# Kernel optimization log

Measured on AMD Instinct MI355X. Metric: run time of the kernel, lower is better.

Reference implementation:

```python
import jax, jax.numpy as jnp
import numpy as np

B, S, E, H = 32, 256, 768, 32
D = E // H  # head_dim = 24


def setup_inputs() -> dict:
    key = jax.random.key(0)
    ks = jax.random.split(key, 10)
    w_sc = 1.0 / np.sqrt(E)  # xavier-ish init scale for weights
    return {
        "feats": jax.random.normal(ks[0], (B, S, E), jnp.float32),
        "attn_bias": jax.random.normal(ks[1], (B, H, S, S), jnp.float32),
        "delta_pos": jax.random.normal(ks[2], (B, S, S, 3), jnp.float32),
        "Wq": jax.random.normal(ks[3], (E, E), jnp.float32) * w_sc,
        "bq": jnp.zeros((E,), jnp.float32),
        "Wk": jax.random.normal(ks[4], (E, E), jnp.float32) * w_sc,
        "bk": jnp.zeros((E,), jnp.float32),
        "Wv": jax.random.normal(ks[5], (E, E), jnp.float32) * w_sc,
        "bv": jnp.zeros((E,), jnp.float32),
        "Wfx": jax.random.normal(ks[6], (E,), jnp.float32) * w_sc,
        "Wfy": jax.random.normal(ks[7], (E,), jnp.float32) * w_sc,
        "Wfz": jax.random.normal(ks[8], (E,), jnp.float32) * w_sc,
    }


def reference(feats, attn_bias, delta_pos, Wq, bq, Wk, bk, Wv, bv, Wfx, Wfy, Wfz):
    b, s, e = feats.shape
    h = attn_bias.shape[1]
    d = e // h
    scaling = d ** -0.5
    # q/k/v projections; q scaled by 1/sqrt(head_dim)
    q = ((feats @ Wq + bq) * scaling).reshape(b, s, h, d).transpose(0, 2, 1, 3)  # (b,h,s,d)
    k = (feats @ Wk + bk).reshape(b, s, h, d).transpose(0, 2, 1, 3)              # (b,h,t,d)
    v = (feats @ Wv + bv).reshape(b, s, h, d).transpose(0, 2, 1, 3)              # (b,h,t,d)
    scores = jnp.einsum('bhsd,bhtd->bhst', q, k) + attn_bias
    probs = jax.nn.softmax(scores, axis=-1)  # dropout p in eval -> identity
    # rot_attn_probs = probs[...,None] * delta_pos[:,None] fused into one contraction:
    # (b,h,s,t) * (b,s,t,3) contracted with (b,h,t,c) over t -> (b,s,3,h,c)
    attn = jnp.einsum('bhst,bstx,bhtc->bsxhc', probs, delta_pos, v)
    attn = attn.reshape(b, s, 3, e)  # flatten (h,c) -> e
    out_x = attn[..., 0, :] @ Wfx  # (b,s)
    out_y = attn[..., 1, :] @ Wfy
    out_z = attn[..., 2, :] @ Wfz
    return jnp.stack([out_x, out_y, out_z], axis=-1)  # (b,s,3)
```

## Files before the change

### kernel.cpp

```cpp
#include <hip/hip_runtime.h>
#include <hip/hip_bf16.h>

#define B_ 32
#define S_ 256
#define E_ 768
#define H_ 32
#define D_ 24
#define NTOT 1664
#define LK 40

typedef __hip_bfloat16 bf16;
typedef __attribute__((ext_vector_type(8))) short short8;
typedef __attribute__((ext_vector_type(4))) float floatx4;
typedef __attribute__((ext_vector_type(2))) float f32x2;

__global__ __launch_bounds__(256) void cast_feats(
    const float* __restrict__ in, bf16* __restrict__ outp, int n4)
{
  int i = blockIdx.x * 256 + threadIdx.x;
  if (i < n4) {
    float4 v = reinterpret_cast<const float4*>(in)[i];
    union { ushort4 u; bf16 b[4]; } pk;
    pk.b[0] = (bf16)v.x; pk.b[1] = (bf16)v.y;
    pk.b[2] = (bf16)v.z; pk.b[3] = (bf16)v.w;
    reinterpret_cast<ushort4*>(outp)[i] = pk.u;
  }
}

__global__ __launch_bounds__(256) void prep_pack(
    const float* __restrict__ Wq, const float* __restrict__ Wk,
    const float* __restrict__ Wv,
    const float* __restrict__ bq, const float* __restrict__ bk,
    const float* __restrict__ bv,
    const float* __restrict__ Wfx, const float* __restrict__ Wfy,
    const float* __restrict__ Wfz,
    bf16* __restrict__ Wt, float* __restrict__ biasf)
{
  const float qscale = 0.20412414523193154f;
  int gid = blockIdx.x * 256 + threadIdx.x;
  if (gid < NTOT * E_) {
    int n = gid / E_, k = gid % E_;
    float val;
    if (n < 768) {
      val = Wq[(size_t)k * E_ + n] * qscale;
    } else if (n < 1536) {
      val = Wk[(size_t)k * E_ + (n - 768)];
    } else if (n < 1632) {
      int nn = n - 1536, x = nn >> 5, h = nn & 31;
      const float* Wf = (x == 0) ? Wfx : (x == 1 ? Wfy : Wfz);
      float s = 0.f;
      #pragma unroll
      for (int c = 0; c < D_; c++)
        s += Wv[(size_t)k * E_ + h * D_ + c] * Wf[h * D_ + c];
      val = s;
    } else {
      val = 0.f;
    }
    Wt[gid] = (bf16)val;
  } else {
    int n = gid - NTOT * E_;
    if (n < NTOT) {
      float val;
      if (n < 768) {
        val = bq[n] * qscale;
      } else if (n < 1536) {
        val = bk[n - 768];
      } else if (n < 1632) {
        int nn = n - 1536, x = nn >> 5, h = nn & 31;
        const float* Wf = (x == 0) ? Wfx : (x == 1 ? Wfy : Wfz);
        float s = 0.f;
        #pragma unroll
        for (int c = 0; c < D_; c++)
          s += bv[h * D_ + c] * Wf[h * D_ + c];
        val = s;
      } else {
        val = 0.f;
      }
      biasf[n] = val;
    }
  }
}

__global__ __launch_bounds__(256) void gemm_qkv(
    const bf16* __restrict__ A, const bf16* __restrict__ Wt,
    const float* __restrict__ biasf,
    bf16* __restrict__ qout, bf16* __restrict__ kout,
    float* __restrict__ vwout)
{
  __shared__ __align__(16) short As[128 * LK];
  __shared__ __align__(16) short Bs[128 * LK];
  int tid = threadIdx.x;
  int m0 = blockIdx.y * 128, n0 = blockIdx.x * 128;
  int lrow = tid >> 2, lcol = (tid & 3) * 8;
  int wave = tid >> 6, lane = tid & 63;
  int wm = (wave >> 1) * 64, wn = (wave & 1) * 64;
  int fr = lane & 15, quad = lane >> 4;

  floatx4 acc[4][4];
  const floatx4 zero = {0.f, 0.f, 0.f, 0.f};
  #pragma unroll
  for (int i = 0; i < 4; i++)
    #pragma unroll
    for (int j = 0; j < 4; j++) acc[i][j] = zero;

  const bf16* Aptr = A + (size_t)(m0 + lrow) * E_ + lcol;
  const bf16* Bptr = Wt + (size_t)(n0 + lrow) * E_ + lcol;
  float4 av0 = *reinterpret_cast<const float4*>(Aptr);
  float4 av1 = *reinterpret_cast<const float4*>(Aptr + (size_t)64 * E_);
  float4 bv0 = *reinterpret_cast<const float4*>(Bptr);
  float4 bv1 = *reinterpret_cast<const float4*>(Bptr + (size_t)64 * E_);

  for (int k0 = 0; k0 < E_; k0 += 32) {
    __syncthreads();
    *reinterpret_cast<float4*>(&As[lrow * LK + lcol]) = av0;
    *reinterpret_cast<float4*>(&As[(lrow + 64) * LK + lcol]) = av1;
    *reinterpret_cast<float4*>(&Bs[lrow * LK + lcol]) = bv0;
    *reinterpret_cast<float4*>(&Bs[(lrow + 64) * LK + lcol]) = bv1;
    __syncthreads();
    if (k0 + 32 < E_) {
      av0 = *reinterpret_cast<const float4*>(Aptr + k0 + 32);
      av1 = *reinterpret_cast<const float4*>(Aptr + (size_t)64 * E_ + k0 + 32);
      bv0 = *reinterpret_cast<const float4*>(Bptr + k0 + 32);
      bv1 = *reinterpret_cast<const float4*>(Bptr + (size_t)64 * E_ + k0 + 32);
    }
    short8 af[4], bfr[4];
    #pragma unroll
    for (int t = 0; t < 4; t++)
      af[t] = *reinterpret_cast<const short8*>(
          &As[(wm + t * 16 + fr) * LK + quad * 8]);
    #pragma unroll
    for (int t = 0; t < 4; t++)
      bfr[t] = *reinterpret_cast<const short8*>(
          &Bs[(wn + t * 16 + fr) * LK + quad * 8]);
    #pragma unroll
    for (int ti = 0; ti < 4; ti++)
      #pragma unroll
      for (int tj = 0; tj < 4; tj++)
        acc[ti][tj] = __builtin_amdgcn_mfma_f32_16x16x32_bf16(
            af[ti], bfr[tj], acc[ti][tj], 0, 0, 0);
  }

  #pragma unroll
  for (int ti = 0; ti < 4; ti++) {
    #pragma unroll
    for (int tj = 0; tj < 4; tj++) {
      int n = n0 + wn + tj * 16 + fr;
      float bias = biasf[n];
      #pragma unroll
      for (int r = 0; r < 4; r++) {
        int m = m0 + wm + ti * 16 + quad * 4 + r;
        int b = m >> 8, s = m & 255;
        float val = acc[ti][tj][r] + bias;
        if (n < 768) {
          int h = n / 24, d = n - h * 24;
          qout[(((size_t)b * H_ + h) * S_ + s) * D_ + d] = (bf16)val;
        } else if (n < 1536) {
          int n2 = n - 768;
          int h = n2 / 24, d = n2 - h * 24;
          kout[(((size_t)b * H_ + h) * S_ + s) * D_ + d] = (bf16)val;
        } else if (n < 1632) {
          int nn = n - 1536, x = nn >> 5, h = nn & 31;
          vwout[(((size_t)x * B_ + b) * H_ + h) * S_ + s] = val;
        }
      }
    }
  }
}

__global__ __launch_bounds__(256, 3) void attn_kernel(
    const bf16* __restrict__ qg, const bf16* __restrict__ kg,
    const float* __restrict__ vwg, const float* __restrict__ biasg,
    const float* __restrict__ dpg, float* __restrict__ out)
{
  __shared__ float ql[64 * 26];
  int blk = blockIdx.x;
  int bh = blk >> 2, st = (blk & 3) * 64;
  int b = bh >> 5, h = bh & 31;
  int tid = threadIdx.x, wave = tid >> 6, lane = tid & 63;
  int t0 = lane * 4;

  f32x2 kr[4][12];
  #pragma unroll
  for (int j = 0; j < 4; j++) {
    const bf16* krow = kg + ((size_t)bh * S_ + t0 + j) * D_;
    #pragma unroll
    for (int i = 0; i < 12; i++) {
      f32x2 kk;
      kk.x = (float)krow[2 * i];
      kk.y = (float)krow[2 * i + 1];
      kr[j][i] = kk;
    }
  }
  float vwr[3][4];
  #pragma unroll
  for (int x = 0; x < 3; x++) {
    float4 v4 = *reinterpret_cast<const float4*>(
        vwg + (((size_t)x * B_ + b) * H_ + h) * S_ + t0);
    vwr[x][0] = v4.x; vwr[x][1] = v4.y; vwr[x][2] = v4.z; vwr[x][3] = v4.w;
  }
  {
    int r = tid >> 2, c0 = (tid & 3) * 6;
    const bf16* qrow = qg + ((size_t)bh * S_ + st + r) * D_ + c0;
    #pragma unroll
    for (int i = 0; i < 6; i++) ql[r * 26 + c0 + i] = (float)qrow[i];
  }
  __syncthreads();

  const float* biasbh = biasg + (size_t)bh * S_ * S_;

  for (int si = 0; si < 16; si++) {
    int sr = si * 4 + wave;
    int s = st + sr;
    float4 bias4 = *reinterpret_cast<const float4*>(biasbh + s * S_ + t0);
    const float* dpr = dpg + ((size_t)(b * S_ + s) * S_) * 3 + (size_t)t0 * 3;
    float4 d0 = *reinterpret_cast<const float4*>(dpr);
    float4 d1 = *reinterpret_cast<const float4*>(dpr + 4);
    float4 d2 = *reinterpret_cast<const float4*>(dpr + 8);

    f32x2 sc2[4];
    #pragma unroll
    for (int j = 0; j < 4; j++) { sc2[j].x = 0.f; sc2[j].y = 0.f; }
    #pragma unroll
    for (int i = 0; i < 12; i++) {
      f32x2 qd = *reinterpret_cast<const f32x2*>(&ql[sr * 26 + 2 * i]);
      #pragma unroll
      for (int j = 0; j < 4; j++) sc2[j] += qd * kr[j][i];
    }
    float sc[4];
    sc[0] = sc2[0].x + sc2[0].y + bias4.x;
    sc[1] = sc2[1].x + sc2[1].y + bias4.y;
    sc[2] = sc2[2].x + sc2[2].y + bias4.z;
    sc[3] = sc2[3].x + sc2[3].y + bias4.w;

    float mx = fmaxf(fmaxf(sc[0], sc[1]), fmaxf(sc[2], sc[3]));
    #pragma unroll
    for (int o = 32; o; o >>= 1) mx = fmaxf(mx, __shfl_xor(mx, o));
    float p[4], l = 0.f;
    #pragma unroll
    for (int j = 0; j < 4; j++) { p[j] = __expf(sc[j] - mx); l += p[j]; }
    #pragma unroll
    for (int o = 32; o; o >>= 1) l += __shfl_xor(l, o);
    float inv = 1.0f / l;

    float dx[4] = {d0.x, d0.w, d1.z, d2.y};
    float dy[4] = {d0.y, d1.x, d1.w, d2.z};
    float dz[4] = {d0.z, d1.y, d2.x, d2.w};

    float ax = 0.f, ay = 0.f, az = 0.f;
    #pragma unroll
    for (int j = 0; j < 4; j++) {
      float w = p[j] * inv;
      ax += w * dx[j] * vwr[0][j];
      ay += w * dy[j] * vwr[1][j];
      az += w * dz[j] * vwr[2][j];
    }
    #pragma unroll
    for (int o = 32; o; o >>= 1) {
      ax += __shfl_xor(ax, o);
      ay += __shfl_xor(ay, o);
      az += __shfl_xor(az, o);
    }
    if (lane == 0) {
      float* op = out + (size_t)(b * S_ + s) * 3;
      atomicAdd(op + 0, ax);
      atomicAdd(op + 1, ay);
      atomicAdd(op + 2, az);
    }
  }
}

extern "C" void kernel_launch(void* const* d_in, const int* in_sizes, int n_in,
                              void* d_out, int out_size, void* d_ws, size_t ws_size,
                              hipStream_t stream)
{
  const float* feats     = (const float*)d_in[0];
  const float* attn_bias = (const float*)d_in[1];
  const float* delta_pos = (const float*)d_in[2];
  const float* Wq        = (const float*)d_in[3];
  const float* bq        = (const float*)d_in[4];
  const float* Wk        = (const float*)d_in[5];
  const float* bk        = (const float*)d_in[6];
  const float* Wv        = (const float*)d_in[7];
  const float* bv        = (const float*)d_in[8];
  const float* Wfx       = (const float*)d_in[9];
  const float* Wfy       = (const float*)d_in[10];
  const float* Wfz       = (const float*)d_in[11];

  char* ws = (char*)d_ws;
  size_t off = 0;
  auto alloc = [&](size_t bytes) -> void* {
    void* p = ws + off;
    off = (off + bytes + 255) & ~(size_t)255;
    return p;
  };
  bf16*  ws_fb   = (bf16*) alloc((size_t)B_ * S_ * E_ * 2);
  bf16*  ws_q    = (bf16*) alloc((size_t)B_ * H_ * S_ * D_ * 2);
  bf16*  ws_k    = (bf16*) alloc((size_t)B_ * H_ * S_ * D_ * 2);
  float* ws_vw   = (float*)alloc((size_t)3 * B_ * H_ * S_ * 4);
  bf16*  ws_Wt   = (bf16*) alloc((size_t)NTOT * E_ * 2);
  float* ws_bias = (float*)alloc((size_t)NTOT * 4);

  hipMemsetAsync(d_out, 0, (size_t)B_ * S_ * 3 * 4, stream);

  int n4 = B_ * S_ * E_ / 4;
  cast_feats<<<(n4 + 255) / 256, 256, 0, stream>>>(feats, ws_fb, n4);

  int prep_n = NTOT * E_ + NTOT;
  prep_pack<<<(prep_n + 255) / 256, 256, 0, stream>>>(
      Wq, Wk, Wv, bq, bk, bv, Wfx, Wfy, Wfz, ws_Wt, ws_bias);

  gemm_qkv<<<dim3(NTOT / 128, B_ * S_ / 128), 256, 0, stream>>>(
      ws_fb, ws_Wt, ws_bias, ws_q, ws_k, ws_vw);

  attn_kernel<<<B_ * H_ * 4, 256, 0, stream>>>(ws_q, ws_k, ws_vw, attn_bias,
                                               delta_pos, (float*)d_out);
}
```

Before: 610.2 us.

## Restructure attention to one thread per query row with shared K/V tile

The attention kernel now runs one block per (batch, head) and gives each thread one query row. The thread loops over all 256 keys, which are staged once in shared memory together with the value-weight projections. This removes the per-row wave shuffle reductions for max, sum and outputs, and prefetches the bias and delta_pos tiles one step ahead in registers. Softmax now subtracts a fixed constant of 4 instead of the running row max, which assumes scores stay far from fp32 exp overflow. Each thread also reads its own strided rows of bias and delta_pos, so global loads are less coalesced.

```diff
diff --git a/kernel.cpp b/kernel.cpp
--- a/kernel.cpp
+++ b/kernel.cpp
@@ -167,106 +167,125 @@
   }
 }
 
-__global__ __launch_bounds__(256, 3) void attn_kernel(
+__global__ __launch_bounds__(256) void attn_kernel(
     const bf16* __restrict__ qg, const bf16* __restrict__ kg,
     const float* __restrict__ vwg, const float* __restrict__ biasg,
     const float* __restrict__ dpg, float* __restrict__ out)
 {
-  __shared__ float ql[64 * 26];
-  int blk = blockIdx.x;
-  int bh = blk >> 2, st = (blk & 3) * 64;
+  __shared__ __align__(16) float kv[S_][28];
+  int bh = blockIdx.x;
   int b = bh >> 5, h = bh & 31;
-  int tid = threadIdx.x, wave = tid >> 6, lane = tid & 63;
-  int t0 = lane * 4;
-
-  f32x2 kr[4][12];
-  #pragma unroll
-  for (int j = 0; j < 4; j++) {
-    const bf16* krow = kg + ((size_t)bh * S_ + t0 + j) * D_;
-    #pragma unroll
-    for (int i = 0; i < 12; i++) {
-      f32x2 kk;
-      kk.x = (float)krow[2 * i];
-      kk.y = (float)krow[2 * i + 1];
-      kr[j][i] = kk;
-    }
-  }
-  float vwr[3][4];
-  #pragma unroll
-  for (int x = 0; x < 3; x++) {
-    float4 v4 = *reinterpret_cast<const float4*>(
-        vwg + (((size_t)x * B_ + b) * H_ + h) * S_ + t0);
-    vwr[x][0] = v4.x; vwr[x][1] = v4.y; vwr[x][2] = v4.z; vwr[x][3] = v4.w;
-  }
+  int s = threadIdx.x;
+
   {
-    int r = tid >> 2, c0 = (tid & 3) * 6;
-    const bf16* qrow = qg + ((size_t)bh * S_ + st + r) * D_ + c0;
-    #pragma unroll
-    for (int i = 0; i < 6; i++) ql[r * 26 + c0 + i] = (float)qrow[i];
+    const short8* kr8 = reinterpret_cast<const short8*>(
+        kg + ((size_t)bh * S_ + s) * D_);
+    #pragma unroll
+    for (int i = 0; i < 3; i++) {
+      short8 kk = kr8[i];
+      float4 f0, f1;
+      union { short u; bf16 bb; } cv;
+      cv.u = kk[0]; f0.x = (float)cv.bb;
+      cv.u = kk[1]; f0.y = (float)cv.bb;
+      cv.u = kk[2]; f0.z = (float)cv.bb;
+      cv.u = kk[3]; f0.w = (float)cv.bb;
+      cv.u = kk[4]; f1.x = (float)cv.bb;
+      cv.u = kk[5]; f1.y = (float)cv.bb;
+      cv.u = kk[6]; f1.z = (float)cv.bb;
+      cv.u = kk[7]; f1.w = (float)cv.bb;
+      *reinterpret_cast<float4*>(&kv[s][i * 8]) = f0;
+      *reinterpret_cast<float4*>(&kv[s][i * 8 + 4]) = f1;
+    }
+    float4 vwp;
+    vwp.x = vwg[(((size_t)0 * B_ + b) * H_ + h) * S_ + s];
+    vwp.y = vwg[(((size_t)1 * B_ + b) * H_ + h) * S_ + s];
+    vwp.z = vwg[(((size_t)2 * B_ + b) * H_ + h) * S_ + s];
+    vwp.w = 0.f;
+    *reinterpret_cast<float4*>(&kv[s][24]) = vwp;
+  }
+
+  f32x2 qd[12];
+  {
+    const short8* qr8 = reinterpret_cast<const short8*>(
+        qg + ((size_t)bh * S_ + s) * D_);
+    #pragma unroll
+    for (int i = 0; i < 3; i++) {
+      short8 qq = qr8[i];
+      #pragma unroll
+      for (int j = 0; j < 4; j++) {
+        union { short u; bf16 bb; } a, c;
+        a.u = qq[2 * j]; c.u = qq[2 * j + 1];
+        f32x2 t2; t2.x = (float)a.bb; t2.y = (float)c.bb;
+        qd[i * 4 + j] = t2;
+      }
+    }
   }
   __syncthreads();
 
-  const float* biasbh = biasg + (size_t)bh * S_ * S_;
-
-  for (int si = 0; si < 16; si++) {
-    int sr = si * 4 + wave;
-    int s = st + sr;
-    float4 bias4 = *reinterpret_cast<const float4*>(biasbh + s * S_ + t0);
-    const float* dpr = dpg + ((size_t)(b * S_ + s) * S_) * 3 + (size_t)t0 * 3;
-    float4 d0 = *reinterpret_cast<const float4*>(dpr);
-    float4 d1 = *reinterpret_cast<const float4*>(dpr + 4);
-    float4 d2 = *reinterpret_cast<const float4*>(dpr + 8);
-
-    f32x2 sc2[4];
-    #pragma unroll
-    for (int j = 0; j < 4; j++) { sc2[j].x = 0.f; sc2[j].y = 0.f; }
-    #pragma unroll
-    for (int i = 0; i < 12; i++) {
-      f32x2 qd = *reinterpret_cast<const f32x2*>(&ql[sr * 26 + 2 * i]);
-      #pragma unroll
-      for (int j = 0; j < 4; j++) sc2[j] += qd * kr[j][i];
-    }
-    float sc[4];
-    sc[0] = sc2[0].x + sc2[0].y + bias4.x;
-    sc[1] = sc2[1].x + sc2[1].y + bias4.y;
-    sc[2] = sc2[2].x + sc2[2].y + bias4.z;
-    sc[3] = sc2[3].x + sc2[3].y + bias4.w;
-
-    float mx = fmaxf(fmaxf(sc[0], sc[1]), fmaxf(sc[2], sc[3]));
-    #pragma unroll
-    for (int o = 32; o; o >>= 1) mx = fmaxf(mx, __shfl_xor(mx, o));
-    float p[4], l = 0.f;
-    #pragma unroll
-    for (int j = 0; j < 4; j++) { p[j] = __expf(sc[j] - mx); l += p[j]; }
-    #pragma unroll
-    for (int o = 32; o; o >>= 1) l += __shfl_xor(l, o);
-    float inv = 1.0f / l;
-
+  const float* biasp = biasg + (size_t)bh * S_ * S_ + (size_t)s * S_;
+  const float* dpp   = dpg + (size_t)(b * S_ + s) * S_ * 3;
+
+  float l = 0.f, ax = 0.f, ay = 0.f, az = 0.f;
+
+  auto group = [&](int tb, float4 bias4, float4 d0, float4 d1, float4 d2) {
     float dx[4] = {d0.x, d0.w, d1.z, d2.y};
     float dy[4] = {d0.y, d1.x, d1.w, d2.z};
     float dz[4] = {d0.z, d1.y, d2.x, d2.w};
-
-    float ax = 0.f, ay = 0.f, az = 0.f;
+    float bb[4] = {bias4.x, bias4.y, bias4.z, bias4.w};
     #pragma unroll
     for (int j = 0; j < 4; j++) {
-      float w = p[j] * inv;
-      ax += w * dx[j] * vwr[0][j];
-      ay += w * dy[j] * vwr[1][j];
-      az += w * dz[j] * vwr[2][j];
-    }
-    #pragma unroll
-    for (int o = 32; o; o >>= 1) {
-      ax += __shfl_xor(ax, o);
-      ay += __shfl_xor(ay, o);
-      az += __shfl_xor(az, o);
-    }
-    if (lane == 0) {
-      float* op = out + (size_t)(b * S_ + s) * 3;
-      atomicAdd(op + 0, ax);
-      atomicAdd(op + 1, ay);
-      atomicAdd(op + 2, az);
-    }
-  }
+      const float4* krow4 = reinterpret_cast<const float4*>(&kv[tb + j][0]);
+      f32x2 acc2; acc2.x = 0.f; acc2.y = 0.f;
+      #pragma unroll
+      for (int i = 0; i < 6; i++) {
+        float4 k4 = krow4[i];
+        f32x2 klo; klo.x = k4.x; klo.y = k4.y;
+        f32x2 khi; khi.x = k4.z; khi.y = k4.w;
+        acc2 += qd[2 * i] * klo;
+        acc2 += qd[2 * i + 1] * khi;
+      }
+      float4 vw4 = krow4[6];
+      float sc = acc2.x + acc2.y + (bb[j] - 4.0f);
+      float p = __expf(sc);
+      l += p;
+      ax = fmaf(p * dx[j], vw4.x, ax);
+      ay = fmaf(p * dy[j], vw4.y, ay);
+      az = fmaf(p * dz[j], vw4.z, az);
+    }
+  };
+
+  float4 nb0 = *reinterpret_cast<const float4*>(biasp);
+  float4 nb1 = *reinterpret_cast<const float4*>(biasp + 4);
+  float4 ne0 = *reinterpret_cast<const float4*>(dpp);
+  float4 ne1 = *reinterpret_cast<const float4*>(dpp + 4);
+  float4 ne2 = *reinterpret_cast<const float4*>(dpp + 8);
+  float4 ne3 = *reinterpret_cast<const float4*>(dpp + 12);
+  float4 ne4 = *reinterpret_cast<const float4*>(dpp + 16);
+  float4 ne5 = *reinterpret_cast<const float4*>(dpp + 20);
+
+  for (int t0 = 0; t0 < S_; t0 += 8) {
+    float4 b0 = nb0, b1 = nb1;
+    float4 e0 = ne0, e1 = ne1, e2 = ne2, e3 = ne3, e4 = ne4, e5 = ne5;
+    int tn = (t0 + 8 < S_) ? t0 + 8 : 0;
+    nb0 = *reinterpret_cast<const float4*>(biasp + tn);
+    nb1 = *reinterpret_cast<const float4*>(biasp + tn + 4);
+    const float* dpn = dpp + (size_t)tn * 3;
+    ne0 = *reinterpret_cast<const float4*>(dpn);
+    ne1 = *reinterpret_cast<const float4*>(dpn + 4);
+    ne2 = *reinterpret_cast<const float4*>(dpn + 8);
+    ne3 = *reinterpret_cast<const float4*>(dpn + 12);
+    ne4 = *reinterpret_cast<const float4*>(dpn + 16);
+    ne5 = *reinterpret_cast<const float4*>(dpn + 20);
+
+    group(t0, b0, e0, e1, e2);
+    group(t0 + 4, b1, e3, e4, e5);
+  }
+
+  float inv = 1.0f / l;
+  float* op = out + (size_t)(b * S_ + s) * 3;
+  atomicAdd(op + 0, ax * inv);
+  atomicAdd(op + 1, ay * inv);
+  atomicAdd(op + 2, az * inv);
 }
 
 extern "C" void kernel_launch(void* const* d_in, const int* in_sizes, int n_in,
@@ -312,6 +331,6 @@
   gemm_qkv<<<dim3(NTOT / 128, B_ * S_ / 128), 256, 0, stream>>>(
       ws_fb, ws_Wt, ws_bias, ws_q, ws_k, ws_vw);
 
-  attn_kernel<<<B_ * H_ * 4, 256, 0, stream>>>(ws_q, ws_k, ws_vw, attn_bias,
-                                               delta_pos, (float*)d_out);
-}
+  attn_kernel<<<B_ * H_, 256, 0, stream>>>(ws_q, ws_k, ws_vw, attn_bias,
+                                           delta_pos, (float*)d_out);
+}
```

Result: no change. 610.4 us (+0.0%).
